# Performance work log

Hardware: AMD Instinct MI355X
Metric: run time of the kernel (lower is better)

Reference implementation:

```python
import jax, jax.numpy as jnp
import numpy as np

ACT_DIM = 768
DICT_SIZE = 32768
S0 = 4096          # top-level latent size (dict_size // prod(lower sizes))
S1 = 8             # lower_level_latent_sizes[0]
K = 64             # per-token top-k (applied globally as k * batch)


def setup_inputs() -> dict:
    key = jax.random.key(0)
    ks = jax.random.split(key, 7)
    scale_e = 1.0 / np.sqrt(ACT_DIM)
    scale_d = 1.0 / np.sqrt(DICT_SIZE)
    return {
        "x": jax.random.normal(ks[0], (4096, ACT_DIM), dtype=jnp.float32),
        "W0": jax.random.normal(ks[1], (S0, ACT_DIM), dtype=jnp.float32) * scale_e,
        "b0": jnp.zeros((S0,), dtype=jnp.float32),
        "W1": jax.random.normal(ks[2], (DICT_SIZE, ACT_DIM), dtype=jnp.float32) * scale_e,
        "b1": jnp.zeros((DICT_SIZE,), dtype=jnp.float32),
        "Wd": jax.random.normal(ks[3], (ACT_DIM, DICT_SIZE), dtype=jnp.float32) * scale_d,
        "b_dec": jnp.zeros((ACT_DIM,), dtype=jnp.float32),
    }


def reference(x, W0, b0, W1, b1, Wd, b_dec):
    B = x.shape[0]
    x_centered = x - b_dec                                   # [B, D]
    # hierarchical relu encoders
    l0 = jax.nn.relu(x_centered @ W0.T + b0)                 # [B, S0]
    l1 = jax.nn.relu(x_centered @ W1.T + b1)                 # [B, S0*S1]
    # multiplicative gating: lower-level gate broadcast over finest level
    final_dense = (l1.reshape(B, S0, S1) * l0[:, :, None]).reshape(B, S0 * S1)
    # global batch top-k over flattened [B * dict_size]
    flat = final_dense.reshape(-1)
    k_for_batch = min(K * B, flat.shape[0])
    vals, idx = jax.lax.top_k(flat, k_for_batch)
    sparse_flat = jnp.zeros_like(flat).at[idx].set(vals)
    encoded = sparse_flat.reshape(B, S0 * S1)
    # decode
    x_hat = encoded @ Wd.T + b_dec                           # [B, D]
    return x_hat
```

## Files before the change

### kernel.cpp

```cpp
#include <hip/hip_runtime.h>
#include <stdint.h>

#define DDIM 768
#define BROWS 4096
#define S0N 4096
#define DICT 32768
#define KTOT 262144u
#define PREF 2.0f
#define DELTA 4e-3f
#define CAND_CAP 8388608u
#define BAND_CAP 4096

static constexpr size_t OFF_XH   = 0;
static constexpr size_t OFF_XL   = 6291456;
static constexpr size_t OFF_W0H  = 12582912;
static constexpr size_t OFF_W0L  = 18874368;
static constexpr size_t OFF_W1H  = 25165824;
static constexpr size_t OFF_W1L  = 75497472;
static constexpr size_t OFF_WDT  = 0;
static constexpr size_t OFF_L0   = 125829120;
static constexpr size_t OFF_CTRL = 192937984;
static constexpr size_t OFF_ROWC = 193069056;
static constexpr size_t OFF_ROWD = 193085440;
static constexpr size_t OFF_CAND = 201474048;
static constexpr size_t WS_NEED  = 268582912;


typedef __attribute__((ext_vector_type(8))) short bf16x8;
typedef __attribute__((ext_vector_type(4))) float f32x4;

__device__ __forceinline__ unsigned umin_(unsigned a, unsigned b) { return a < b ? a : b; }
__device__ __forceinline__ float relu_(float v) { return v > 0.f ? v : 0.f; }

__device__ __forceinline__ unsigned short f2bf(float f) {
    union { float f; unsigned u; } v; v.f = f;
    unsigned r = v.u + 0x7FFFu + ((v.u >> 16) & 1u);
    return (unsigned short)(r >> 16);
}
__device__ __forceinline__ float bf2f(unsigned short h) {
    union { float f; unsigned u; } v; v.u = ((unsigned)h) << 16;
    return v.f;
}
__device__ __forceinline__ void split1(float a, short& h, short& l) {
    unsigned short hb = f2bf(a);
    float rem = a - bf2f(hb);
    h = (short)hb;
    l = (short)f2bf(rem);
}

__device__ __forceinline__ void gl16(const void* g, void* l) {
    __builtin_amdgcn_global_load_lds(
        (const __attribute__((address_space(1))) void*)g,
        (__attribute__((address_space(3))) void*)l,
        16, 0, 0);
}

__global__ void k_split_x(const float* __restrict__ x, const float* __restrict__ b_dec,
                          short* __restrict__ XH, short* __restrict__ XL) {
    int i = blockIdx.x * 256 + threadIdx.x;
    float4 xv = ((const float4*)x)[i];
    int d = (i % (DDIM / 4)) * 4;
    float4 bv = *(const float4*)(b_dec + d);
    float a[4] = {xv.x - bv.x, xv.y - bv.y, xv.z - bv.z, xv.w - bv.w};
    short4 h, lo;
    split1(a[0], h.x, lo.x); split1(a[1], h.y, lo.y);
    split1(a[2], h.z, lo.z); split1(a[3], h.w, lo.w);
    ((short4*)XH)[i] = h;
    ((short4*)XL)[i] = lo;
}

__global__ void k_split_w(const float* __restrict__ W, short* __restrict__ H,
                          short* __restrict__ L) {
    int i = blockIdx.x * 256 + threadIdx.x;
    float4 wv = ((const float4*)W)[i];
    short4 h, lo;
    split1(wv.x, h.x, lo.x); split1(wv.y, h.y, lo.y);
    split1(wv.z, h.z, lo.z); split1(wv.w, h.w, lo.w);
    ((short4*)H)[i] = h;
    ((short4*)L)[i] = lo;
}

__global__ void k_transpose(const float* __restrict__ Wd, float* __restrict__ WdT) {
    __shared__ float tile[32][33];
    int j0 = blockIdx.x * 32, d0 = blockIdx.y * 32;
    int tx = threadIdx.x & 31, ty = threadIdx.x >> 5;
#pragma unroll
    for (int i = 0; i < 4; ++i)
        tile[ty + i * 8][tx] = Wd[(size_t)(d0 + ty + i * 8) * DICT + j0 + tx];
    __syncthreads();
#pragma unroll
    for (int i = 0; i < 4; ++i)
        WdT[(size_t)(j0 + ty + i * 8) * DDIM + d0 + tx] = tile[tx][ty + i * 8];
}

template<int EPI>
__launch_bounds__(512, 2) __global__
void k_mm(const short* __restrict__ XH, const short* __restrict__ XL,
          const short* __restrict__ WH, const short* __restrict__ WL,
          const float* __restrict__ bias, float* __restrict__ l0buf,
          uint2* __restrict__ cand, unsigned* __restrict__ ctrl) {
    __shared__ __align__(16) char smem[131072];

    const int t = threadIdx.x;
    const int w = t >> 6, l = t & 63;
    const int wm = w >> 2, wn = w & 3;
    const int lr = l & 15, lk = l >> 4;

    const int nwg = gridDim.x;
    const int bid = blockIdx.x;
    const int swz = (bid & 7) * (nwg >> 3) + (bid >> 3);
    const int bm = (swz & 15) << 8;
    const int bn = (swz >> 4) << 8;

    const int a0 = 2 * w, a1 = a0 + 1;
    const unsigned aB0 = (unsigned)(bm + (a0 >> 3) * 128 + (a0 & 7) * 16 + lr) * 768u + (unsigned)(lk * 8);
    const unsigned aB1 = (unsigned)(bm + (a1 >> 3) * 128 + (a1 & 7) * 16 + lr) * 768u + (unsigned)(lk * 8);
    const unsigned bB0 = (unsigned)(bn + (a0 >> 2) * 64 + (a0 & 3) * 16 + lr) * 768u + (unsigned)(lk * 8);
    const unsigned bB1 = (unsigned)(bn + (a1 >> 2) * 64 + (a1 & 3) * 16 + lr) * 768u + (unsigned)(lk * 8);

    f32x4 acc[8][4];
#pragma unroll
    for (int i = 0; i < 8; ++i)
#pragma unroll
        for (int j = 0; j < 4; ++j) acc[i][j] = (f32x4){0.f, 0.f, 0.f, 0.f};

#pragma unroll
    for (int J = 0; J < 3; ++J) {
        const unsigned kb = (unsigned)J * 32u;
        char* dA = smem + J * 16384 + a0 * 1024;
        char* dB = smem + 65536 + J * 16384 + a0 * 1024;
        gl16(XH + aB0 + kb, dA);
        gl16(XH + aB1 + kb, dA + 1024);
        gl16(WH + bB0 + kb, dB);
        gl16(WH + bB1 + kb, dB + 1024);
    }

#pragma unroll 1
    for (int H = 0; H < 72; ++H) {
        if (H < 70)       asm volatile("s_waitcnt vmcnt(8)" ::: "memory");
        else if (H == 70) asm volatile("s_waitcnt vmcnt(4)" ::: "memory");
        else              asm volatile("s_waitcnt vmcnt(0)" ::: "memory");
        __builtin_amdgcn_s_barrier();

        const char* rA = smem + (H & 3) * 16384;
        const char* rB = smem + 65536 + (H & 3) * 16384;

        const int J = H + 3;
        const short* As = XH; const short* Bs = WH; unsigned kb = 0;
        char* dA = nullptr; char* dB = nullptr;
        const bool hj = J < 72;
        if (hj) {
            const int ktJ = J >> 1;
            if (ktJ < 12)      { As = XH; Bs = WH; kb = (unsigned)ktJ * 64u; }
            else if (ktJ < 24) { As = XH; Bs = WL; kb = (unsigned)(ktJ - 12) * 64u; }
            else               { As = XL; Bs = WH; kb = (unsigned)(ktJ - 24) * 64u; }
            kb += (unsigned)(J & 1) * 32u;
            dA = smem + (J & 3) * 16384 + a0 * 1024;
            dB = smem + 65536 + (J & 3) * 16384 + a0 * 1024;
        }

        bf16x8 bfr[4], af[4];
#pragma unroll
        for (int nj = 0; nj < 4; ++nj)
            bfr[nj] = *(const bf16x8*)(rB + (wn * 4 + nj) * 1024 + l * 16);
#pragma unroll
        for (int m2 = 0; m2 < 4; ++m2)
            af[m2] = *(const bf16x8*)(rA + (wm * 8 + m2) * 1024 + l * 16);
        if (hj) { gl16(As + aB0 + kb, dA); gl16(As + aB1 + kb, dA + 1024); }
        __builtin_amdgcn_s_setprio(1);
#pragma unroll
        for (int m2 = 0; m2 < 4; ++m2)
#pragma unroll
            for (int nj = 0; nj < 4; ++nj)
                acc[m2][nj] = __builtin_amdgcn_mfma_f32_16x16x32_bf16(
                    af[m2], bfr[nj], acc[m2][nj], 0, 0, 0);
        __builtin_amdgcn_s_setprio(0);

#pragma unroll
        for (int m2 = 0; m2 < 4; ++m2)
            af[m2] = *(const bf16x8*)(rA + (wm * 8 + 4 + m2) * 1024 + l * 16);
        if (hj) { gl16(Bs + bB0 + kb, dB); gl16(Bs + bB1 + kb, dB + 1024); }
        __builtin_amdgcn_s_setprio(1);
#pragma unroll
        for (int m2 = 0; m2 < 4; ++m2)
#pragma unroll
            for (int nj = 0; nj < 4; ++nj)
                acc[4 + m2][nj] = __builtin_amdgcn_mfma_f32_16x16x32_bf16(
                    af[m2], bfr[nj], acc[4 + m2][nj], 0, 0, 0);
        __builtin_amdgcn_s_setprio(0);
    }
    __syncthreads();

    if constexpr (EPI == 0) {
#pragma unroll
        for (int mi = 0; mi < 8; ++mi) {
#pragma unroll
            for (int r = 0; r < 4; ++r) {
                const int row = bm + wm * 128 + mi * 16 + lk * 4 + r;
                float* orow = l0buf + (size_t)row * S0N;
#pragma unroll
                for (int nj = 0; nj < 4; ++nj) {
                    const int col = bn + wn * 64 + nj * 16 + lr;
                    orow[col] = relu_(acc[mi][nj][r] + bias[col]);
                }
            }
        }
    } else {
        unsigned* pscan = (unsigned*)smem;
        unsigned cnt = 0;
#pragma unroll
        for (int mi = 0; mi < 8; ++mi)
#pragma unroll
            for (int nj = 0; nj < 4; ++nj)
#pragma unroll
                for (int r = 0; r < 4; ++r) {
                    const int row = bm + wm * 128 + mi * 16 + lk * 4 + r;
                    const int col = bn + wn * 64 + nj * 16 + lr;
                    float v = relu_(acc[mi][nj][r] + bias[col]);
                    v *= l0buf[(size_t)row * S0N + (col >> 3)];
                    acc[mi][nj][r] = v;
                    cnt += (v >= PREF) ? 1u : 0u;
                }
        pscan[t] = cnt;
        __syncthreads();
        for (int s = 1; s < 512; s <<= 1) {
            unsigned v2 = (t >= s) ? pscan[t - s] : 0u;
            __syncthreads();
            pscan[t] += v2;
            __syncthreads();
        }
        if (t == 511) pscan[512] = atomicAdd(&ctrl[0], pscan[511]);
        __syncthreads();
        unsigned off = pscan[512] + pscan[t] - cnt;
#pragma unroll
        for (int mi = 0; mi < 8; ++mi)
#pragma unroll
            for (int nj = 0; nj < 4; ++nj)
#pragma unroll
                for (int r = 0; r < 4; ++r) {
                    const float v = acc[mi][nj][r];
                    if (v >= PREF) {
                        const int row = bm + wm * 128 + mi * 16 + lk * 4 + r;
                        const int col = bn + wn * 64 + nj * 16 + lr;
                        if (off < CAND_CAP)
                            cand[off] = make_uint2(__float_as_uint(v),
                                                   ((unsigned)row << 15) | (unsigned)col);
                        ++off;
                    }
                }
    }
}

__global__ void k_hist1(const uint2* __restrict__ cand, unsigned* __restrict__ ctrl) {
    __shared__ unsigned h[2048];
    for (int i = threadIdx.x; i < 2048; i += 256) h[i] = 0;
    __syncthreads();
    unsigned n = umin_(ctrl[0], CAND_CAP);
    for (unsigned i = blockIdx.x * 256 + threadIdx.x; i < n; i += gridDim.x * 256)
        atomicAdd(&h[cand[i].x >> 20], 1u);
    __syncthreads();
    unsigned* hist = ctrl + 256;
    for (int i = threadIdx.x; i < 2048; i += 256)
        if (h[i]) atomicAdd(&hist[i], h[i]);
}

__global__ void k_scan1(unsigned* __restrict__ ctrl) {
    __shared__ unsigned hs[2048];
    __shared__ unsigned cs[256];
    const unsigned* h = ctrl + 256;
    int t = threadIdx.x;
    for (int i = t; i < 2048; i += 256) hs[i] = h[i];
    __syncthreads();
    unsigned s = 0;
    for (int b = 0; b < 8; ++b) s += hs[t * 8 + b];
    cs[t] = s;
    __syncthreads();
    if (t == 0) {
        unsigned cum = 0, T = 0, cb = 0;
        for (int c = 255; c >= 0; --c) {
            if (cum + cs[c] >= KTOT) {
                for (int b = c * 8 + 7; b >= c * 8; --b) {
                    cum += hs[b];
                    if (cum >= KTOT) { T = (unsigned)b; cb = cum - hs[b]; break; }
                }
                break;
            }
            cum += cs[c];
        }
        ctrl[1] = T; ctrl[2] = cb;
    }
}

__global__ void k_hist2(const uint2* __restrict__ cand, unsigned* __restrict__ ctrl) {
    unsigned n = umin_(ctrl[0], CAND_CAP);
    unsigned T = ctrl[1];
    unsigned* hist2 = ctrl + 2304;
    for (unsigned i = blockIdx.x * 256 + threadIdx.x; i < n; i += gridDim.x * 256) {
        unsigned u = cand[i].x;
        if ((u >> 20) == T) atomicAdd(&hist2[(u >> 8) & 0xFFFu], 1u);
    }
}

__global__ void k_scan2(unsigned* __restrict__ ctrl) {
    __shared__ unsigned hs[4096];
    __shared__ unsigned cs[256];
    const unsigned* h = ctrl + 2304;
    int t = threadIdx.x;
    for (int i = t; i < 4096; i += 256) hs[i] = h[i];
    __syncthreads();
    unsigned s = 0;
    for (int b = 0; b < 16; ++b) s += hs[t * 16 + b];
    cs[t] = s;
    __syncthreads();
    if (t == 0) {
        unsigned cum = ctrl[2], T2 = 0;
        for (int c = 255; c >= 0; --c) {
            if (cum + cs[c] >= KTOT) {
                for (int b = c * 16 + 15; b >= c * 16; --b) {
                    cum += hs[b];
                    if (cum >= KTOT) { T2 = (unsigned)b; break; }
                }
                break;
            }
            cum += cs[c];
        }
        ctrl[3] = (ctrl[1] << 12) | T2;
    }
}

__global__ void k_band(const uint2* __restrict__ cand, unsigned* __restrict__ ctrl) {
    __shared__ unsigned lhi;
    if (threadIdx.x == 0) lhi = 0;
    __syncthreads();
    unsigned n = umin_(ctrl[0], CAND_CAP);
    unsigned H = ctrl[3];
    float lo = __uint_as_float(H << 8) - DELTA;
    float hi = __uint_as_float((H + 1u) << 8) + DELTA;
    unsigned* band_idx = ctrl + 6400;
    unsigned my = 0;
    for (unsigned i = blockIdx.x * 256 + threadIdx.x; i < n; i += gridDim.x * 256) {
        float v = __uint_as_float(cand[i].x);
        if (v > hi) ++my;
        else if (v >= lo) {
            unsigned p = atomicAdd(&ctrl[5], 1u);
            if (p < BAND_CAP) band_idx[p] = cand[i].y;
        }
    }
    atomicAdd(&lhi, my);
    __syncthreads();
    if (threadIdx.x == 0 && lhi) atomicAdd(&ctrl[4], lhi);
}

__global__ void k_f64(const float* __restrict__ x, const float* __restrict__ b_dec,
                      const float* __restrict__ W0, const float* __restrict__ b0,
                      const float* __restrict__ W1, const float* __restrict__ b1,
                      const unsigned* __restrict__ ctrl, double* __restrict__ band_v) {
    unsigned n = umin_(ctrl[5], BAND_CAP);
    unsigned bi = blockIdx.x;
    if (bi >= n) return;
    const unsigned* band_idx = ctrl + 6400;
    unsigned idx = band_idx[bi];
    int b = idx >> 15, j = idx & 32767, s0 = j >> 3;
    int lane = threadIdx.x;
    const float* xr = x + (size_t)b * DDIM;
    const float* w1 = W1 + (size_t)j * DDIM;
    const float* w0 = W0 + (size_t)s0 * DDIM;
    double d1 = 0.0, d0 = 0.0;
    for (int k = lane; k < DDIM; k += 64) {
        double xv = (double)xr[k] - (double)b_dec[k];
        d1 += xv * (double)w1[k];
        d0 += xv * (double)w0[k];
    }
    for (int off = 32; off; off >>= 1) {
        d1 += __shfl_down(d1, off);
        d0 += __shfl_down(d0, off);
    }
    if (lane == 0) {
        double l1v = d1 + (double)b1[j];  l1v = l1v > 0.0 ? l1v : 0.0;
        double l0v = d0 + (double)b0[s0]; l0v = l0v > 0.0 ? l0v : 0.0;
        band_v[bi] = l1v * l0v;
    }
}

__global__ void k_final(unsigned* __restrict__ ctrl, const double* __restrict__ band_v,
                        uint2* __restrict__ extra) {
    __shared__ unsigned long long skey[BAND_CAP];
    __shared__ unsigned sidx[BAND_CAP];
    int t = threadIdx.x;
    unsigned n = umin_(ctrl[5], BAND_CAP);
    const unsigned* band_idx = ctrl + 6400;
    for (int i = t; i < BAND_CAP; i += 256) {
        if ((unsigned)i < n) {
            skey[i] = (unsigned long long)__double_as_longlong(band_v[i]);
            sidx[i] = band_idx[i];
        } else {
            skey[i] = 0ull; sidx[i] = 0xFFFFFFFFu;
        }
    }
    __syncthreads();
    for (int kk = 2; kk <= BAND_CAP; kk <<= 1) {
        for (int jj = kk >> 1; jj > 0; jj >>= 1) {
            for (int i = t; i < BAND_CAP; i += 256) {
                int ixj = i ^ jj;
                if (ixj > i) {
                    unsigned long long ka = skey[i], kb = skey[ixj];
                    unsigned ia = sidx[i], ib = sidx[ixj];
                    bool ab = (ka > kb) || (ka == kb && ia < ib);
                    bool asc = ((i & kk) == 0);
                    if (asc ? !ab : ab) {
                        skey[i] = kb; skey[ixj] = ka;
                        sidx[i] = ib; sidx[ixj] = ia;
                    }
                }
            }
            __syncthreads();
        }
    }
    unsigned c_hi = ctrl[4];
    unsigned k_rem = (c_hi < KTOT) ? (KTOT - c_hi) : 0u;
    if (k_rem > n) k_rem = n;
    if (t == 0) ctrl[6] = k_rem;
    for (unsigned i = t; i < k_rem; i += 256)
        extra[i] = make_uint2(sidx[i],
                              __float_as_uint((float)__longlong_as_double((long long)skey[i])));
}

__global__ void k_rows_a(const uint2* __restrict__ cand, const unsigned* __restrict__ ctrl,
                         unsigned* __restrict__ rowc, uint2* __restrict__ rowd) {
    unsigned n = umin_(ctrl[0], CAND_CAP);
    unsigned H = ctrl[3];
    float hi = __uint_as_float((H + 1u) << 8) + DELTA;
    for (unsigned i = blockIdx.x * 256 + threadIdx.x; i < n; i += gridDim.x * 256) {
        unsigned u = cand[i].x;
        if (__uint_as_float(u) > hi) {
            unsigned idx = cand[i].y;
            unsigned b = idx >> 15;
            unsigned p = atomicAdd(&rowc[b], 1u);
            if (p < 256u) rowd[(b << 8) + p] = make_uint2(idx & 32767u, u);
        }
    }
}

__global__ void k_rows_b(const unsigned* __restrict__ ctrl, const uint2* __restrict__ extra,
                         unsigned* __restrict__ rowc, uint2* __restrict__ rowd) {
    unsigned k_rem = ctrl[6];
    for (unsigned i = blockIdx.x * 256 + threadIdx.x; i < k_rem; i += gridDim.x * 256) {
        unsigned idx = extra[i].x;
        unsigned b = idx >> 15;
        unsigned p = atomicAdd(&rowc[b], 1u);
        if (p < 256u) rowd[(b << 8) + p] = make_uint2(idx & 32767u, extra[i].y);
    }
}

__launch_bounds__(256) __global__
void k_decode(const uint2* __restrict__ rowd, const unsigned* __restrict__ rowc,
              const float* __restrict__ WdT, const float* __restrict__ b_dec,
              float* __restrict__ out) {
    __shared__ uint2 e[256];
    int b = blockIdx.x, t = threadIdx.x;
    unsigned c = rowc[b]; if (c > 256u) c = 256u;
    if ((unsigned)t < c) e[t] = rowd[(b << 8) + t];
    __syncthreads();
    float a0 = b_dec[t], a1 = b_dec[t + 256], a2 = b_dec[t + 512];
#pragma unroll 4
    for (unsigned i = 0; i < c; ++i) {
        float v = __uint_as_float(e[i].y);
        const float* w = WdT + (size_t)e[i].x * DDIM;
        a0 = fmaf(v, w[t], a0);
        a1 = fmaf(v, w[t + 256], a1);
        a2 = fmaf(v, w[t + 512], a2);
    }
    float* o = out + (size_t)b * DDIM;
    o[t] = a0; o[t + 256] = a1; o[t + 512] = a2;
}

extern "C" void kernel_launch(void* const* d_in, const int* in_sizes, int n_in,
                              void* d_out, int out_size, void* d_ws, size_t ws_size,
                              hipStream_t stream) {
    const float* x     = (const float*)d_in[0];
    const float* W0    = (const float*)d_in[1];
    const float* b0    = (const float*)d_in[2];
    const float* W1    = (const float*)d_in[3];
    const float* b1    = (const float*)d_in[4];
    const float* Wd    = (const float*)d_in[5];
    const float* b_dec = (const float*)d_in[6];
    float* out = (float*)d_out;

    if (ws_size < WS_NEED) {
        hipMemsetAsync(d_out, 0, (size_t)out_size * sizeof(float), stream);
        return;
    }

    char* ws = (char*)d_ws;
    short*    XH     = (short*)(ws + OFF_XH);
    short*    XL     = (short*)(ws + OFF_XL);
    short*    W0H    = (short*)(ws + OFF_W0H);
    short*    W0L    = (short*)(ws + OFF_W0L);
    short*    W1H    = (short*)(ws + OFF_W1H);
    short*    W1L    = (short*)(ws + OFF_W1L);
    float*    WdT    = (float*)(ws + OFF_WDT);
    float*    l0     = (float*)(ws + OFF_L0);
    unsigned* ctrl   = (unsigned*)(ws + OFF_CTRL);
    double*   band_v = (double*)(ws + OFF_CTRL + 65536);
    uint2*    extra  = (uint2*)(ws + OFF_CTRL + 98304);
    unsigned* rowc   = (unsigned*)(ws + OFF_ROWC);
    uint2*    rowd   = (uint2*)(ws + OFF_ROWD);
    uint2*    cand   = (uint2*)(ws + OFF_CAND);

    hipMemsetAsync(ctrl, 0, 6400 * sizeof(unsigned), stream);
    hipMemsetAsync(rowc, 0, BROWS * sizeof(unsigned), stream);

    k_split_x<<<(BROWS * DDIM / 4) / 256, 256, 0, stream>>>(x, b_dec, XH, XL);
    k_split_w<<<(S0N * DDIM / 4) / 256, 256, 0, stream>>>(W0, W0H, W0L);
    k_split_w<<<(DICT * DDIM / 4) / 256, 256, 0, stream>>>(W1, W1H, W1L);

    k_mm<0><<<(S0N / 256) * 16, 512, 0, stream>>>(XH, XL, W0H, W0L, b0, l0, nullptr, nullptr);
    k_mm<1><<<(DICT / 256) * 16, 512, 0, stream>>>(XH, XL, W1H, W1L, b1, l0, cand, ctrl);

    k_transpose<<<dim3(DICT / 32, DDIM / 32), 256, 0, stream>>>(Wd, WdT);

    k_hist1<<<1024, 256, 0, stream>>>(cand, ctrl);
    k_scan1<<<1, 256, 0, stream>>>(ctrl);
    k_hist2<<<1024, 256, 0, stream>>>(cand, ctrl);
    k_scan2<<<1, 256, 0, stream>>>(ctrl);
    k_band<<<1024, 256, 0, stream>>>(cand, ctrl);
    k_f64<<<BAND_CAP, 64, 0, stream>>>(x, b_dec, W0, b0, W1, b1, ctrl, band_v);
    k_final<<<1, 256, 0, stream>>>(ctrl, band_v, extra);

    k_rows_a<<<1024, 256, 0, stream>>>(cand, ctrl, rowc, rowd);
    k_rows_b<<<32, 256, 0, stream>>>(ctrl, extra, rowc, rowd);
    k_decode<<<BROWS, 256, 0, stream>>>(rowd, rowc, WdT, b_dec, out);
}
```

Baseline: 1.207 ms.

## Use bf16 decoder weights, fuse row scatter into band pass, add MFMA loop barriers

The transposed decoder weight matrix is now stored as bf16, and the decode kernel reads four bf16 values per thread with 192 threads and vector stores. This halves the bytes of the gathered weight traffic. The row-scatter pass that re-read the candidate buffer is folded into the band kernel, removing one full pass over the candidates. The GEMM inner loop gains explicit workgroup barriers and LDS waits around the MFMA blocks to synchronise waves. This adds sync cost and lowers decode precision, which could affect tolerance.

```diff
diff --git a/kernel.cpp b/kernel.cpp
--- a/kernel.cpp
+++ b/kernel.cpp
@@ -80,7 +80,7 @@
     ((short4*)L)[i] = lo;
 }
 
-__global__ void k_transpose(const float* __restrict__ Wd, float* __restrict__ WdT) {
+__global__ void k_transpose(const float* __restrict__ Wd, unsigned short* __restrict__ WdT) {
     __shared__ float tile[32][33];
     int j0 = blockIdx.x * 32, d0 = blockIdx.y * 32;
     int tx = threadIdx.x & 31, ty = threadIdx.x >> 5;
@@ -90,7 +90,7 @@
     __syncthreads();
 #pragma unroll
     for (int i = 0; i < 4; ++i)
-        WdT[(size_t)(j0 + ty + i * 8) * DDIM + d0 + tx] = tile[tx][ty + i * 8];
+        WdT[(size_t)(j0 + ty + i * 8) * DDIM + d0 + tx] = f2bf(tile[tx][ty + i * 8]);
 }
 
 template<int EPI>
@@ -167,6 +167,10 @@
         for (int m2 = 0; m2 < 4; ++m2)
             af[m2] = *(const bf16x8*)(rA + (wm * 8 + m2) * 1024 + l * 16);
         if (hj) { gl16(As + aB0 + kb, dA); gl16(As + aB1 + kb, dA + 1024); }
+        __builtin_amdgcn_sched_barrier(0);
+        __builtin_amdgcn_s_barrier();
+        asm volatile("s_waitcnt lgkmcnt(0)" ::: "memory");
+        __builtin_amdgcn_sched_barrier(0);
         __builtin_amdgcn_s_setprio(1);
 #pragma unroll
         for (int m2 = 0; m2 < 4; ++m2)
@@ -175,11 +179,16 @@
                 acc[m2][nj] = __builtin_amdgcn_mfma_f32_16x16x32_bf16(
                     af[m2], bfr[nj], acc[m2][nj], 0, 0, 0);
         __builtin_amdgcn_s_setprio(0);
+        __builtin_amdgcn_s_barrier();
 
 #pragma unroll
         for (int m2 = 0; m2 < 4; ++m2)
             af[m2] = *(const bf16x8*)(rA + (wm * 8 + 4 + m2) * 1024 + l * 16);
         if (hj) { gl16(Bs + bB0 + kb, dB); gl16(Bs + bB1 + kb, dB + 1024); }
+        __builtin_amdgcn_sched_barrier(0);
+        __builtin_amdgcn_s_barrier();
+        asm volatile("s_waitcnt lgkmcnt(0)" ::: "memory");
+        __builtin_amdgcn_sched_barrier(0);
         __builtin_amdgcn_s_setprio(1);
 #pragma unroll
         for (int m2 = 0; m2 < 4; ++m2)
@@ -188,6 +197,7 @@
                 acc[4 + m2][nj] = __builtin_amdgcn_mfma_f32_16x16x32_bf16(
                     af[m2], bfr[nj], acc[4 + m2][nj], 0, 0, 0);
         __builtin_amdgcn_s_setprio(0);
+        __builtin_amdgcn_s_barrier();
     }
     __syncthreads();
 
@@ -328,7 +338,8 @@
     }
 }
 
-__global__ void k_band(const uint2* __restrict__ cand, unsigned* __restrict__ ctrl) {
+__global__ void k_band_rows(const uint2* __restrict__ cand, unsigned* __restrict__ ctrl,
+                            unsigned* __restrict__ rowc, uint2* __restrict__ rowd) {
     __shared__ unsigned lhi;
     if (threadIdx.x == 0) lhi = 0;
     __syncthreads();
@@ -339,11 +350,16 @@
     unsigned* band_idx = ctrl + 6400;
     unsigned my = 0;
     for (unsigned i = blockIdx.x * 256 + threadIdx.x; i < n; i += gridDim.x * 256) {
-        float v = __uint_as_float(cand[i].x);
-        if (v > hi) ++my;
-        else if (v >= lo) {
+        uint2 cv = cand[i];
+        float v = __uint_as_float(cv.x);
+        if (v > hi) {
+            ++my;
+            unsigned b = cv.y >> 15;
+            unsigned p = atomicAdd(&rowc[b], 1u);
+            if (p < 256u) rowd[(b << 8) + p] = make_uint2(cv.y & 32767u, cv.x);
+        } else if (v >= lo) {
             unsigned p = atomicAdd(&ctrl[5], 1u);
-            if (p < BAND_CAP) band_idx[p] = cand[i].y;
+            if (p < BAND_CAP) band_idx[p] = cv.y;
         }
     }
     atomicAdd(&lhi, my);
@@ -425,22 +441,6 @@
                               __float_as_uint((float)__longlong_as_double((long long)skey[i])));
 }
 
-__global__ void k_rows_a(const uint2* __restrict__ cand, const unsigned* __restrict__ ctrl,
-                         unsigned* __restrict__ rowc, uint2* __restrict__ rowd) {
-    unsigned n = umin_(ctrl[0], CAND_CAP);
-    unsigned H = ctrl[3];
-    float hi = __uint_as_float((H + 1u) << 8) + DELTA;
-    for (unsigned i = blockIdx.x * 256 + threadIdx.x; i < n; i += gridDim.x * 256) {
-        unsigned u = cand[i].x;
-        if (__uint_as_float(u) > hi) {
-            unsigned idx = cand[i].y;
-            unsigned b = idx >> 15;
-            unsigned p = atomicAdd(&rowc[b], 1u);
-            if (p < 256u) rowd[(b << 8) + p] = make_uint2(idx & 32767u, u);
-        }
-    }
-}
-
 __global__ void k_rows_b(const unsigned* __restrict__ ctrl, const uint2* __restrict__ extra,
                          unsigned* __restrict__ rowc, uint2* __restrict__ rowd) {
     unsigned k_rem = ctrl[6];
@@ -452,26 +452,26 @@
     }
 }
 
-__launch_bounds__(256) __global__
+__launch_bounds__(192) __global__
 void k_decode(const uint2* __restrict__ rowd, const unsigned* __restrict__ rowc,
-              const float* __restrict__ WdT, const float* __restrict__ b_dec,
+              const unsigned short* __restrict__ WdT, const float* __restrict__ b_dec,
               float* __restrict__ out) {
     __shared__ uint2 e[256];
     int b = blockIdx.x, t = threadIdx.x;
     unsigned c = rowc[b]; if (c > 256u) c = 256u;
-    if ((unsigned)t < c) e[t] = rowd[(b << 8) + t];
-    __syncthreads();
-    float a0 = b_dec[t], a1 = b_dec[t + 256], a2 = b_dec[t + 512];
+    for (int i = t; i < (int)c; i += 192) e[i] = rowd[(b << 8) + i];
+    __syncthreads();
+    float4 a = *(const float4*)(b_dec + 4 * t);
 #pragma unroll 4
     for (unsigned i = 0; i < c; ++i) {
         float v = __uint_as_float(e[i].y);
-        const float* w = WdT + (size_t)e[i].x * DDIM;
-        a0 = fmaf(v, w[t], a0);
-        a1 = fmaf(v, w[t + 256], a1);
-        a2 = fmaf(v, w[t + 512], a2);
-    }
-    float* o = out + (size_t)b * DDIM;
-    o[t] = a0; o[t + 256] = a1; o[t + 512] = a2;
+        ushort4 w4 = *(const ushort4*)(WdT + (size_t)e[i].x * DDIM + 4 * t);
+        a.x = fmaf(v, bf2f(w4.x), a.x);
+        a.y = fmaf(v, bf2f(w4.y), a.y);
+        a.z = fmaf(v, bf2f(w4.z), a.z);
+        a.w = fmaf(v, bf2f(w4.w), a.w);
+    }
+    *(float4*)(out + (size_t)b * DDIM + 4 * t) = a;
 }
 
 extern "C" void kernel_launch(void* const* d_in, const int* in_sizes, int n_in,
@@ -492,20 +492,20 @@
     }
 
     char* ws = (char*)d_ws;
-    short*    XH     = (short*)(ws + OFF_XH);
-    short*    XL     = (short*)(ws + OFF_XL);
-    short*    W0H    = (short*)(ws + OFF_W0H);
-    short*    W0L    = (short*)(ws + OFF_W0L);
-    short*    W1H    = (short*)(ws + OFF_W1H);
-    short*    W1L    = (short*)(ws + OFF_W1L);
-    float*    WdT    = (float*)(ws + OFF_WDT);
-    float*    l0     = (float*)(ws + OFF_L0);
-    unsigned* ctrl   = (unsigned*)(ws + OFF_CTRL);
-    double*   band_v = (double*)(ws + OFF_CTRL + 65536);
-    uint2*    extra  = (uint2*)(ws + OFF_CTRL + 98304);
-    unsigned* rowc   = (unsigned*)(ws + OFF_ROWC);
-    uint2*    rowd   = (uint2*)(ws + OFF_ROWD);
-    uint2*    cand   = (uint2*)(ws + OFF_CAND);
+    short*          XH     = (short*)(ws + OFF_XH);
+    short*          XL     = (short*)(ws + OFF_XL);
+    short*          W0H    = (short*)(ws + OFF_W0H);
+    short*          W0L    = (short*)(ws + OFF_W0L);
+    short*          W1H    = (short*)(ws + OFF_W1H);
+    short*          W1L    = (short*)(ws + OFF_W1L);
+    unsigned short* WdT    = (unsigned short*)(ws + OFF_WDT);
+    float*          l0     = (float*)(ws + OFF_L0);
+    unsigned*       ctrl   = (unsigned*)(ws + OFF_CTRL);
+    double*         band_v = (double*)(ws + OFF_CTRL + 65536);
+    uint2*          extra  = (uint2*)(ws + OFF_CTRL + 98304);
+    unsigned*       rowc   = (unsigned*)(ws + OFF_ROWC);
+    uint2*          rowd   = (uint2*)(ws + OFF_ROWD);
+    uint2*          cand   = (uint2*)(ws + OFF_CAND);
 
     hipMemsetAsync(ctrl, 0, 6400 * sizeof(unsigned), stream);
     hipMemsetAsync(rowc, 0, BROWS * sizeof(unsigned), stream);
@@ -523,11 +523,10 @@
     k_scan1<<<1, 256, 0, stream>>>(ctrl);
     k_hist2<<<1024, 256, 0, stream>>>(cand, ctrl);
     k_scan2<<<1, 256, 0, stream>>>(ctrl);
-    k_band<<<1024, 256, 0, stream>>>(cand, ctrl);
+    k_band_rows<<<1024, 256, 0, stream>>>(cand, ctrl, rowc, rowd);
     k_f64<<<BAND_CAP, 64, 0, stream>>>(x, b_dec, W0, b0, W1, b1, ctrl, band_v);
     k_final<<<1, 256, 0, stream>>>(ctrl, band_v, extra);
-
-    k_rows_a<<<1024, 256, 0, stream>>>(cand, ctrl, rowc, rowd);
     k_rows_b<<<32, 256, 0, stream>>>(ctrl, extra, rowc, rowd);
-    k_decode<<<BROWS, 256, 0, stream>>>(rowd, rowc, WdT, b_dec, out);
-}
+
+    k_decode<<<BROWS, 192, 0, stream>>>(rowd, rowc, WdT, b_dec, out);
+}
```

After: 1.143 ms. -5.2%, faster.
